# Optimization experiments

Hardware: AMD Instinct MI355X
Metric: run time of the kernel (lower is better)

Reference implementation:

```python
import jax, jax.numpy as jnp
import numpy as np

HARDNESS = 5.0

def setup_inputs() -> dict:
    key = jax.random.key(0)
    k1, k2 = jax.random.split(key)
    x = jax.random.normal(k1, (64, 8, 32, 32, 16), dtype=jnp.float32)
    ref = jax.random.normal(k2, (64, 16), dtype=jnp.float32)
    return {"input": x, "ref": ref}

def reference(input, ref):
    # Squared L2 distance from every element vector (last dim) to every codeword,
    x2 = jnp.sum(input * input, axis=-1)                      # (D1,D2,D3,D4)
    r2 = jnp.sum(ref * ref, axis=-1)                          # (M,)
    cross = jnp.einsum('abcde,me->mabcd', input, ref)         # (M,D1,D2,D3,D4)
    sq_l2 = x2[None] - 2.0 * cross + r2[:, None, None, None, None]
    # Softmax over codebook axis with -hardness temperature (dim=0 in torch).
    y = jax.nn.softmax(-HARDNESS * sq_l2, axis=0)             # (M,D1,D2,D3,D4)
    # Weighted combination of codewords.
    z = jnp.einsum('mabcd,me->abcde', y, ref)                 # (D1..D5)
    return z
```

## Files before the change

kernel.cpp:

```cpp
#include <hip/hip_runtime.h>
#include <math.h>

#define CB_M 64
#define CB_D 16
#define HARD 5.0f
#define LOG2E 1.44269504088896340736f
#define SSTRIDE 68

typedef __attribute__((ext_vector_type(8))) short bf16x8;
typedef __attribute__((ext_vector_type(4))) float f32x4;
typedef __attribute__((ext_vector_type(4))) int   i32x4;

#if __has_builtin(__builtin_amdgcn_exp2f)
#define EXP2F(x) __builtin_amdgcn_exp2f(x)
#else
#define EXP2F(x) exp2f(x)
#endif

#if __has_builtin(__builtin_amdgcn_rcpf)
#define RCPF(x) __builtin_amdgcn_rcpf(x)
#else
#define RCPF(x) (1.0f / (x))
#endif

__device__ __forceinline__ ushort f2bf_rne(float f) {
    unsigned u = __float_as_uint(f);
    u += 0x7fffu + ((u >> 16) & 1u);
    return (ushort)(u >> 16);
}
__device__ __forceinline__ float bf2f(ushort h) {
    return __uint_as_float(((unsigned)h) << 16);
}
__device__ __forceinline__ int pk(float a, float b) {
    return (int)__builtin_amdgcn_perm(__float_as_uint(a), __float_as_uint(b), 0x07060302u);
}
__device__ __forceinline__ float rnd(float a) {
    return __uint_as_float(__float_as_uint(a) + 0x8000u);
}
__device__ __forceinline__ float hi_trunc(float a) {
    return __uint_as_float(__float_as_uint(a) & 0xffff0000u);
}

__global__ __launch_bounds__(256, 2) void stq_main(const float* __restrict__ x,
                                                   const float* __restrict__ ref,
                                                   float* __restrict__ out,
                                                   int ntiles) {
    __shared__ __align__(16) float  cb_bias[CB_M];
    __shared__ __align__(16) ushort cb_rs_hi[CB_M][CB_D];
    __shared__ __align__(16) ushort cb_rs_lo[CB_M][CB_D];
    __shared__ __align__(16) ushort cb_rzT_hi[CB_D][CB_M];
    __shared__ __align__(16) ushort cb_rzT_lo[CB_D][CB_M];
    __shared__ __align__(16) float  slds[4][16 * SSTRIDE];

    const int tid = threadIdx.x;

    if (tid < CB_M) {
        const f32x4* rp = (const f32x4*)(ref + tid * CB_D);
        f32x4 q0 = rp[0], q1 = rp[1], q2 = rp[2], q3 = rp[3];
        float r[CB_D] = {q0.x,q0.y,q0.z,q0.w, q1.x,q1.y,q1.z,q1.w,
                         q2.x,q2.y,q2.z,q2.w, q3.x,q3.y,q3.z,q3.w};
        float r2 = 0.0f;
#pragma unroll
        for (int j = 0; j < CB_D; ++j) r2 += r[j] * r[j];
        cb_bias[tid] = -(HARD * LOG2E) * r2;
        const float s = 2.0f * HARD * LOG2E;
#pragma unroll
        for (int j = 0; j < CB_D; ++j) {
            float v = s * r[j];
            ushort h = f2bf_rne(v);
            cb_rs_hi[tid][j] = h;
            cb_rs_lo[tid][j] = f2bf_rne(v - bf2f(h));
            ushort zh = f2bf_rne(r[j]);
            cb_rzT_hi[j][tid] = zh;
            cb_rzT_lo[j][tid] = f2bf_rne(r[j] - bf2f(zh));
        }
    }
    __syncthreads();

    const int lane = tid & 63;
    const int wid  = tid >> 6;
    const int i = lane & 15;
    const int c = lane >> 4;
    const bool wantlo = (c >= 2);
    float* S = slds[wid];

    bf16x8 BsH[4], BsL[4];
    f32x4  cinit[4];
#pragma unroll
    for (int t = 0; t < 4; ++t) {
        float b = cb_bias[16 * t + i];
        cinit[t] = (f32x4){b, b, b, b};
        BsH[t] = *(const bf16x8*)&cb_rs_hi[16 * t + i][(c & 1) * 8];
        BsL[t] = *(const bf16x8*)&cb_rs_lo[16 * t + i][(c & 1) * 8];
    }
    bf16x8 BzH0 = *(const bf16x8*)&cb_rzT_hi[i][c * 8];
    bf16x8 BzH1 = *(const bf16x8*)&cb_rzT_hi[i][32 + c * 8];
    bf16x8 BzL0 = *(const bf16x8*)&cb_rzT_lo[i][c * 8];
    bf16x8 BzL1 = *(const bf16x8*)&cb_rzT_lo[i][32 + c * 8];

    const int nwaves = gridDim.x * 4;
    int tile = blockIdx.x * 4 + wid;

    f32x4 nxa, nxb;
    {
        const float* xp = x + ((size_t)tile * 16 + i) * CB_D + (c & 1) * 8;
        nxa = *(const f32x4*)xp;
        nxb = *(const f32x4*)(xp + 4);
    }

#pragma unroll 1
    for (; tile < ntiles; tile += nwaves) {
        f32x4 xa = nxa, xb = nxb;
        const int nt = tile + nwaves;
        if (nt < ntiles) {
            const float* xp = x + ((size_t)nt * 16 + i) * CB_D + (c & 1) * 8;
            nxa = *(const f32x4*)xp;
            nxb = *(const f32x4*)(xp + 4);
        }

        i32x4 Ahi, Alo;
        Ahi.x = pk(xa.y, xa.x); Ahi.y = pk(xa.w, xa.z);
        Ahi.z = pk(xb.y, xb.x); Ahi.w = pk(xb.w, xb.z);
        float l0 = xa.x - hi_trunc(xa.x), l1 = xa.y - hi_trunc(xa.y);
        float l2 = xa.z - hi_trunc(xa.z), l3 = xa.w - hi_trunc(xa.w);
        float l4 = xb.x - hi_trunc(xb.x), l5 = xb.y - hi_trunc(xb.y);
        float l6 = xb.z - hi_trunc(xb.z), l7 = xb.w - hi_trunc(xb.w);
        Alo.x = pk(rnd(l1), rnd(l0)); Alo.y = pk(rnd(l3), rnd(l2));
        Alo.z = pk(rnd(l5), rnd(l4)); Alo.w = pk(rnd(l7), rnd(l6));
        i32x4 Ai;
        Ai.x = wantlo ? Alo.x : Ahi.x;
        Ai.y = wantlo ? Alo.y : Ahi.y;
        Ai.z = wantlo ? Alo.z : Ahi.z;
        Ai.w = wantlo ? Alo.w : Ahi.w;
        bf16x8 A = __builtin_bit_cast(bf16x8, Ai);

        f32x4 acc[4];
#pragma unroll
        for (int t = 0; t < 4; ++t) {
            acc[t] = __builtin_amdgcn_mfma_f32_16x16x32_bf16(A, BsH[t], cinit[t], 0, 0, 0);
            acc[t] = __builtin_amdgcn_mfma_f32_16x16x32_bf16(A, BsL[t], acc[t], 0, 0, 0);
        }

#pragma unroll
        for (int t = 0; t < 4; ++t)
#pragma unroll
            for (int r = 0; r < 4; ++r)
                S[(4 * c + r) * SSTRIDE + i + 16 * t] = acc[t][r];

        float sv[16];
        {
            const f32x4* p0 = (const f32x4*)(S + i * SSTRIDE + c * 8);
            const f32x4* p1 = (const f32x4*)(S + i * SSTRIDE + 32 + c * 8);
            f32x4 a0 = p0[0], a1 = p0[1], b0 = p1[0], b1 = p1[1];
            sv[0]=a0.x; sv[1]=a0.y; sv[2]=a0.z; sv[3]=a0.w;
            sv[4]=a1.x; sv[5]=a1.y; sv[6]=a1.z; sv[7]=a1.w;
            sv[8]=b0.x; sv[9]=b0.y; sv[10]=b0.z; sv[11]=b0.w;
            sv[12]=b1.x; sv[13]=b1.y; sv[14]=b1.z; sv[15]=b1.w;
        }

        float lmax = sv[0];
#pragma unroll
        for (int j = 1; j < 16; ++j) lmax = fmaxf(lmax, sv[j]);
        lmax = fmaxf(lmax, __shfl_xor(lmax, 16, 64));
        lmax = fmaxf(lmax, __shfl_xor(lmax, 32, 64));

        float e[16];
        float lsum = 0.0f;
#pragma unroll
        for (int j = 0; j < 16; ++j) { e[j] = EXP2F(sv[j] - lmax); lsum += e[j]; }
        lsum += __shfl_xor(lsum, 16, 64);
        lsum += __shfl_xor(lsum, 32, 64);
        const float inv = RCPF(lsum);

        i32x4 P1i, P2i;
        P1i.x = pk(rnd(e[1] * inv),  rnd(e[0] * inv));
        P1i.y = pk(rnd(e[3] * inv),  rnd(e[2] * inv));
        P1i.z = pk(rnd(e[5] * inv),  rnd(e[4] * inv));
        P1i.w = pk(rnd(e[7] * inv),  rnd(e[6] * inv));
        P2i.x = pk(rnd(e[9] * inv),  rnd(e[8] * inv));
        P2i.y = pk(rnd(e[11] * inv), rnd(e[10] * inv));
        P2i.z = pk(rnd(e[13] * inv), rnd(e[12] * inv));
        P2i.w = pk(rnd(e[15] * inv), rnd(e[14] * inv));
        bf16x8 P1 = __builtin_bit_cast(bf16x8, P1i);
        bf16x8 P2 = __builtin_bit_cast(bf16x8, P2i);

        f32x4 cz = {0.0f, 0.0f, 0.0f, 0.0f};
        cz = __builtin_amdgcn_mfma_f32_16x16x32_bf16(P1, BzH0, cz, 0, 0, 0);
        cz = __builtin_amdgcn_mfma_f32_16x16x32_bf16(P2, BzH1, cz, 0, 0, 0);
        cz = __builtin_amdgcn_mfma_f32_16x16x32_bf16(P1, BzL0, cz, 0, 0, 0);
        cz = __builtin_amdgcn_mfma_f32_16x16x32_bf16(P2, BzL1, cz, 0, 0, 0);

        const int rowbase = tile * 16;
#pragma unroll
        for (int r = 0; r < 4; ++r)
            out[(size_t)(rowbase + 4 * c + r) * CB_D + i] = cz[r];
    }
}

extern "C" void kernel_launch(void* const* d_in, const int* in_sizes, int n_in,
                              void* d_out, int out_size, void* d_ws, size_t ws_size,
                              hipStream_t stream) {
    const float* x   = (const float*)d_in[0];
    const float* ref = (const float*)d_in[1];
    float* out = (float*)d_out;

    const int nvec = in_sizes[0] / CB_D;
    const int ntiles = nvec / 16;

    stq_main<<<1024, 256, 0, stream>>>(x, ref, out, ntiles);
}
```

Before: 89.70 us.

## Transpose first MFMA so score fragments land in softmax layout, drop LDS round-trip

Swaps the operand roles in the distance MFMA, making codewords the A operand with a permuted row order and x the B operand. Each lane's accumulator fragment then matches the layout the second MFMA expects for the probabilities, so the per-wave LDS scatter and gather is removed. The second GEMM also splits into two independent accumulators to shorten the MFMA dependency chain. The permuted codeword indexing and bias layout are intricate, so any indexing mistake would break correctness.

```diff
diff --git a/kernel.cpp b/kernel.cpp
--- a/kernel.cpp
+++ b/kernel.cpp
@@ -5,7 +5,6 @@
 #define CB_D 16
 #define HARD 5.0f
 #define LOG2E 1.44269504088896340736f
-#define SSTRIDE 68
 
 typedef __attribute__((ext_vector_type(8))) short bf16x8;
 typedef __attribute__((ext_vector_type(4))) float f32x4;
@@ -50,7 +49,6 @@
     __shared__ __align__(16) ushort cb_rs_lo[CB_M][CB_D];
     __shared__ __align__(16) ushort cb_rzT_hi[CB_D][CB_M];
     __shared__ __align__(16) ushort cb_rzT_lo[CB_D][CB_M];
-    __shared__ __align__(16) float  slds[4][16 * SSTRIDE];
 
     const int tid = threadIdx.x;
 
@@ -81,17 +79,21 @@
     const int wid  = tid >> 6;
     const int i = lane & 15;
     const int c = lane >> 4;
-    const bool wantlo = (c >= 2);
-    float* S = slds[wid];
 
-    bf16x8 BsH[4], BsL[4];
+    bf16x8 A1[4], A2[4];
     f32x4  cinit[4];
+    bf16x8 zfrag;
+#pragma unroll
+    for (int j = 0; j < 8; ++j) zfrag[j] = 0;
 #pragma unroll
     for (int t = 0; t < 4; ++t) {
-        float b = cb_bias[16 * t + i];
-        cinit[t] = (f32x4){b, b, b, b};
-        BsH[t] = *(const bf16x8*)&cb_rs_hi[16 * t + i][(c & 1) * 8];
-        BsL[t] = *(const bf16x8*)&cb_rs_lo[16 * t + i][(c & 1) * 8];
+        const int cwa = 32 * (t >> 1) + 8 * (i >> 2) + 4 * (t & 1) + (i & 3);
+        const ushort* src = (c < 2) ? &cb_rs_hi[cwa][0] : &cb_rs_lo[cwa][0];
+        A1[t] = *(const bf16x8*)(src + (c & 1) * 8);
+        A2[t] = (c < 2) ? A1[t] : zfrag;
+#pragma unroll
+        for (int r = 0; r < 4; ++r)
+            cinit[t][r] = cb_bias[32 * (t >> 1) + 8 * c + 4 * (t & 1) + r];
     }
     bf16x8 BzH0 = *(const bf16x8*)&cb_rzT_hi[i][c * 8];
     bf16x8 BzH1 = *(const bf16x8*)&cb_rzT_hi[i][32 + c * 8];
@@ -118,82 +120,66 @@
             nxb = *(const f32x4*)(xp + 4);
         }
 
-        i32x4 Ahi, Alo;
-        Ahi.x = pk(xa.y, xa.x); Ahi.y = pk(xa.w, xa.z);
-        Ahi.z = pk(xb.y, xb.x); Ahi.w = pk(xb.w, xb.z);
+        i32x4 B1i, B2i;
+        B1i.x = pk(xa.y, xa.x); B1i.y = pk(xa.w, xa.z);
+        B1i.z = pk(xb.y, xb.x); B1i.w = pk(xb.w, xb.z);
         float l0 = xa.x - hi_trunc(xa.x), l1 = xa.y - hi_trunc(xa.y);
         float l2 = xa.z - hi_trunc(xa.z), l3 = xa.w - hi_trunc(xa.w);
         float l4 = xb.x - hi_trunc(xb.x), l5 = xb.y - hi_trunc(xb.y);
         float l6 = xb.z - hi_trunc(xb.z), l7 = xb.w - hi_trunc(xb.w);
-        Alo.x = pk(rnd(l1), rnd(l0)); Alo.y = pk(rnd(l3), rnd(l2));
-        Alo.z = pk(rnd(l5), rnd(l4)); Alo.w = pk(rnd(l7), rnd(l6));
-        i32x4 Ai;
-        Ai.x = wantlo ? Alo.x : Ahi.x;
-        Ai.y = wantlo ? Alo.y : Ahi.y;
-        Ai.z = wantlo ? Alo.z : Ahi.z;
-        Ai.w = wantlo ? Alo.w : Ahi.w;
-        bf16x8 A = __builtin_bit_cast(bf16x8, Ai);
+        B2i.x = pk(rnd(l1), rnd(l0)); B2i.y = pk(rnd(l3), rnd(l2));
+        B2i.z = pk(rnd(l5), rnd(l4)); B2i.w = pk(rnd(l7), rnd(l6));
+        bf16x8 B1 = __builtin_bit_cast(bf16x8, B1i);
+        bf16x8 B2 = __builtin_bit_cast(bf16x8, B2i);
 
         f32x4 acc[4];
 #pragma unroll
         for (int t = 0; t < 4; ++t) {
-            acc[t] = __builtin_amdgcn_mfma_f32_16x16x32_bf16(A, BsH[t], cinit[t], 0, 0, 0);
-            acc[t] = __builtin_amdgcn_mfma_f32_16x16x32_bf16(A, BsL[t], acc[t], 0, 0, 0);
+            acc[t] = __builtin_amdgcn_mfma_f32_16x16x32_bf16(A1[t], B1, cinit[t], 0, 0, 0);
+            acc[t] = __builtin_amdgcn_mfma_f32_16x16x32_bf16(A2[t], B2, acc[t], 0, 0, 0);
         }
 
+        float lmax = acc[0][0];
 #pragma unroll
         for (int t = 0; t < 4; ++t)
 #pragma unroll
-            for (int r = 0; r < 4; ++r)
-                S[(4 * c + r) * SSTRIDE + i + 16 * t] = acc[t][r];
-
-        float sv[16];
-        {
-            const f32x4* p0 = (const f32x4*)(S + i * SSTRIDE + c * 8);
-            const f32x4* p1 = (const f32x4*)(S + i * SSTRIDE + 32 + c * 8);
-            f32x4 a0 = p0[0], a1 = p0[1], b0 = p1[0], b1 = p1[1];
-            sv[0]=a0.x; sv[1]=a0.y; sv[2]=a0.z; sv[3]=a0.w;
-            sv[4]=a1.x; sv[5]=a1.y; sv[6]=a1.z; sv[7]=a1.w;
-            sv[8]=b0.x; sv[9]=b0.y; sv[10]=b0.z; sv[11]=b0.w;
-            sv[12]=b1.x; sv[13]=b1.y; sv[14]=b1.z; sv[15]=b1.w;
-        }
-
-        float lmax = sv[0];
-#pragma unroll
-        for (int j = 1; j < 16; ++j) lmax = fmaxf(lmax, sv[j]);
+            for (int r = 0; r < 4; ++r) lmax = fmaxf(lmax, acc[t][r]);
         lmax = fmaxf(lmax, __shfl_xor(lmax, 16, 64));
         lmax = fmaxf(lmax, __shfl_xor(lmax, 32, 64));
 
-        float e[16];
+        float e[4][4];
         float lsum = 0.0f;
 #pragma unroll
-        for (int j = 0; j < 16; ++j) { e[j] = EXP2F(sv[j] - lmax); lsum += e[j]; }
+        for (int t = 0; t < 4; ++t)
+#pragma unroll
+            for (int r = 0; r < 4; ++r) { e[t][r] = EXP2F(acc[t][r] - lmax); lsum += e[t][r]; }
         lsum += __shfl_xor(lsum, 16, 64);
         lsum += __shfl_xor(lsum, 32, 64);
         const float inv = RCPF(lsum);
 
         i32x4 P1i, P2i;
-        P1i.x = pk(rnd(e[1] * inv),  rnd(e[0] * inv));
-        P1i.y = pk(rnd(e[3] * inv),  rnd(e[2] * inv));
-        P1i.z = pk(rnd(e[5] * inv),  rnd(e[4] * inv));
-        P1i.w = pk(rnd(e[7] * inv),  rnd(e[6] * inv));
-        P2i.x = pk(rnd(e[9] * inv),  rnd(e[8] * inv));
-        P2i.y = pk(rnd(e[11] * inv), rnd(e[10] * inv));
-        P2i.z = pk(rnd(e[13] * inv), rnd(e[12] * inv));
-        P2i.w = pk(rnd(e[15] * inv), rnd(e[14] * inv));
+        P1i.x = pk(rnd(e[0][1] * inv), rnd(e[0][0] * inv));
+        P1i.y = pk(rnd(e[0][3] * inv), rnd(e[0][2] * inv));
+        P1i.z = pk(rnd(e[1][1] * inv), rnd(e[1][0] * inv));
+        P1i.w = pk(rnd(e[1][3] * inv), rnd(e[1][2] * inv));
+        P2i.x = pk(rnd(e[2][1] * inv), rnd(e[2][0] * inv));
+        P2i.y = pk(rnd(e[2][3] * inv), rnd(e[2][2] * inv));
+        P2i.z = pk(rnd(e[3][1] * inv), rnd(e[3][0] * inv));
+        P2i.w = pk(rnd(e[3][3] * inv), rnd(e[3][2] * inv));
         bf16x8 P1 = __builtin_bit_cast(bf16x8, P1i);
         bf16x8 P2 = __builtin_bit_cast(bf16x8, P2i);
 
-        f32x4 cz = {0.0f, 0.0f, 0.0f, 0.0f};
-        cz = __builtin_amdgcn_mfma_f32_16x16x32_bf16(P1, BzH0, cz, 0, 0, 0);
-        cz = __builtin_amdgcn_mfma_f32_16x16x32_bf16(P2, BzH1, cz, 0, 0, 0);
-        cz = __builtin_amdgcn_mfma_f32_16x16x32_bf16(P1, BzL0, cz, 0, 0, 0);
-        cz = __builtin_amdgcn_mfma_f32_16x16x32_bf16(P2, BzL1, cz, 0, 0, 0);
+        f32x4 z0 = {0.0f, 0.0f, 0.0f, 0.0f};
+        f32x4 z1 = {0.0f, 0.0f, 0.0f, 0.0f};
+        z0 = __builtin_amdgcn_mfma_f32_16x16x32_bf16(P1, BzH0, z0, 0, 0, 0);
+        z1 = __builtin_amdgcn_mfma_f32_16x16x32_bf16(P1, BzL0, z1, 0, 0, 0);
+        z0 = __builtin_amdgcn_mfma_f32_16x16x32_bf16(P2, BzH1, z0, 0, 0, 0);
+        z1 = __builtin_amdgcn_mfma_f32_16x16x32_bf16(P2, BzL1, z1, 0, 0, 0);
 
         const int rowbase = tile * 16;
 #pragma unroll
         for (int r = 0; r < 4; ++r)
-            out[(size_t)(rowbase + 4 * c + r) * CB_D + i] = cz[r];
+            out[(size_t)(rowbase + 4 * c + r) * CB_D + i] = z0[r] + z1[r];
     }
 }
 
```

Result: no change. 88.74 us (-1.1%).
